# Kernel tuning notes

Measured on AMD Instinct MI355X. Metric: run time of the kernel, lower is better.

The kernel has to match this reference:

```python
import jax, jax.numpy as jnp
import numpy as np

NEG_INF = -jnp.inf


def setup_inputs() -> dict:
    key = jax.random.key(0)
    k1, k2, k3, k4 = jax.random.split(key, 4)
    B, V = 256, 128000
    logits = jax.random.normal(k1, (B, V), dtype=jnp.float32)
    temperatures = jax.random.uniform(k2, (B,), dtype=jnp.float32, minval=0.5, maxval=1.5)
    top_ks = jax.random.randint(k3, (B,), 0, 1024, dtype=jnp.int32)
    top_ps = jax.random.uniform(k4, (B,), dtype=jnp.float32)
    return {"logits": logits, "temperatures": temperatures, "top_ks": top_ks, "top_ps": top_ps}


def _filtered_logits(logits, temperatures, top_ks, top_ps):
    # Faithful vectorized version of the per-row torch loops.
    B, V = logits.shape
    x = logits.astype(jnp.float32) / temperatures[:, None]

    # Sort each row descending once; reuse for top-k and top-p.
    order = jnp.argsort(-x, axis=-1)                       # [B, V] desc indices
    sorted_x = jnp.take_along_axis(x, order, axis=-1)      # [B, V]
    ranks = jnp.arange(V)[None, :]                         # [1, V]

    # top-k: active only when 0 < k < V (matches torch branch)
    k = top_ks[:, None].astype(jnp.int32)
    topk_active = (k > 0) & (k < V)
    keep_k = jnp.where(topk_active, ranks < k, True)
    sorted_x = jnp.where(keep_k, sorted_x, NEG_INF)

    # top-p on softmax of top-k-filtered logits. Softmax is order-preserving,
    # so sorted probs == softmax of sorted (filtered) logits.
    sorted_probs = jax.nn.softmax(sorted_x, axis=-1)
    cumsum = jnp.cumsum(sorted_probs, axis=-1)
    p = top_ps[:, None]
    cutoff = jnp.sum(cumsum <= p, axis=-1, keepdims=True)  # (cumsum<=p).sum()
    cutoff = jnp.where(cutoff < V, cutoff + 1, cutoff)     # include next token
    topp_active = (p > 0.0) & (p < 1.0)
    keep_p = jnp.where(topp_active, ranks < cutoff, True)
    sorted_x = jnp.where(keep_p, sorted_x, NEG_INF)

    # Unsort back to original token order.
    inv = jnp.argsort(order, axis=-1)
    return jnp.take_along_axis(sorted_x, inv, axis=-1)


def reference(logits, temperatures, top_ks, top_ps):
    x = _filtered_logits(logits, temperatures, top_ks, top_ps)
    probs = jax.nn.softmax(x, axis=-1)
    # Gumbel-max style sampling: argmax(probs / Exp(1)) (torch .exponential_ trick)
    e = jax.random.exponential(jax.random.key(42), probs.shape, dtype=jnp.float32)
    e = jnp.maximum(e, 1e-10)
    return jnp.argmax(probs / e, axis=-1)
```

## Files before the change

kernel.cpp:

```cpp
#include <hip/hip_runtime.h>
#include <stdint.h>

#define VV 128000
#define BLOCK 1024
#define NB 4096
#define CAP 4096
#define THR 2.0f
#define U0  0xC0000000u
#define MSEL 2048

typedef unsigned long long ull;

__device__ __forceinline__ uint32_t rotl32(uint32_t x, int r){ return (x << r) | (x >> (32 - r)); }

__device__ __forceinline__ float exp_noise(uint32_t f){
  const uint32_t ks0 = 0u, ks1 = 42u, ks2 = 0x1BD11BDAu ^ 0u ^ 42u;
  uint32_t x0 = 0u + ks0;
  uint32_t x1 = f + ks1;
#define R1(r) { x0 += x1; x1 = rotl32(x1, r); x1 ^= x0; }
  R1(13) R1(15) R1(26) R1(6)   x0 += ks1; x1 += ks2 + 1u;
  R1(17) R1(29) R1(16) R1(24)  x0 += ks2; x1 += ks0 + 2u;
  R1(13) R1(15) R1(26) R1(6)   x0 += ks0; x1 += ks1 + 3u;
  R1(17) R1(29) R1(16) R1(24)  x0 += ks1; x1 += ks2 + 4u;
  R1(13) R1(15) R1(26) R1(6)   x0 += ks2; x1 += ks0 + 5u;
#undef R1
  uint32_t bits = x0 ^ x1;
  float u = __uint_as_float((bits >> 9) | 0x3F800000u) - 1.0f;
  float e = -log1pf(-u);
  return fmaxf(e, 1e-10f);
}

__device__ __forceinline__ uint32_t fkey(float x){
  uint32_t u = __float_as_uint(x);
  return u ^ ((u & 0x80000000u) ? 0xFFFFFFFFu : 0x80000000u);
}
__device__ __forceinline__ float keyval(uint32_t k){
  uint32_t bits = (k & 0x80000000u) ? (k ^ 0x80000000u) : ~k;
  return __uint_as_float(bits);
}

__device__ void suffix_scan_u(uint32_t* h, uint32_t* tmp, int tid){
  const int base = tid * 4;
  uint32_t l0=h[base], l1=h[base+1], l2=h[base+2], l3=h[base+3];
  uint32_t s3=l3, s2=l2+s3, s1=l1+s2, s0=l0+s1;
  tmp[tid] = s0; __syncthreads();
  for (int d=1; d<BLOCK; d<<=1){
    uint32_t add = (tid+d<BLOCK) ? tmp[tid+d] : 0u;
    __syncthreads();
    tmp[tid] += add;
    __syncthreads();
  }
  uint32_t E = (tid+1<BLOCK) ? tmp[tid+1] : 0u;
  h[base]=s0+E; h[base+1]=s1+E; h[base+2]=s2+E; h[base+3]=s3+E;
  __syncthreads();
}
__device__ void suffix_scan_f(float* h, float* tmp, int tid){
  const int base = tid * 4;
  float l0=h[base], l1=h[base+1], l2=h[base+2], l3=h[base+3];
  float s3=l3, s2=l2+s3, s1=l1+s2, s0=l0+s1;
  tmp[tid] = s0; __syncthreads();
  for (int d=1; d<BLOCK; d<<=1){
    float add = (tid+d<BLOCK) ? tmp[tid+d] : 0.f;
    __syncthreads();
    tmp[tid] += add;
    __syncthreads();
  }
  float E = (tid+1<BLOCK) ? tmp[tid+1] : 0.f;
  h[base]=s0+E; h[base+1]=s1+E; h[base+2]=s2+E; h[base+3]=s3+E;
  __syncthreads();
}

__device__ uint32_t select_tth_smallest(uint32_t* a, int n, int t){
  for (int i=0;i<t;i++){
    int mi=i; uint32_t mv=a[i];
    for (int j=i+1;j<n;j++) if (a[j]<mv){ mv=a[j]; mi=j; }
    a[mi]=a[i]; a[i]=mv;
  }
  return a[t-1];
}

__device__ void bitonic_sort(ull* a, int N, int tid){
  for (int len=2; len<=N; len<<=1){
    for (int j=len>>1; j>0; j>>=1){
      for (int i=tid; i<N; i+=BLOCK){
        int l = i ^ j;
        if (l > i){
          ull x = a[i], y = a[l];
          bool asc = ((i & len) == 0);
          if (asc ? (x > y) : (x < y)){ a[i]=y; a[l]=x; }
        }
      }
      __syncthreads();
    }
  }
}

#define ROW4R_BEGIN \
    for (int c0 = tid; c0 < VV/4; c0 += BLOCK*4){ \
      float4 qv[4]; int cb[4]; bool gv[4]; \
      _Pragma("unroll") \
      for (int t=0;t<4;t++){ int cc = c0 + t*BLOCK; gv[t] = (cc < VV/4); cb[t] = cc*4; if (gv[t]) qv[t] = rp[cc]; } \
      _Pragma("unroll") \
      for (int t=0;t<4;t++) if (gv[t]){ \
        float vs[4] = {qv[t].x, qv[t].y, qv[t].z, qv[t].w}; \
        _Pragma("unroll") \
        for (int j=0;j<4;j++){ \
          uint32_t u = fkey(vs[j]); \
          uint32_t idx = (uint32_t)(cb[t]+j); \
          (void)idx;
#define ROW4R_END } } }

#define ROW4_BEGIN \
    for (int c0 = tid; c0 < VV/4; c0 += BLOCK*4){ \
      float4 qv[4]; int cb[4]; bool gv[4]; \
      _Pragma("unroll") \
      for (int t=0;t<4;t++){ int cc = c0 + t*BLOCK; gv[t] = (cc < VV/4); cb[t] = cc*4; if (gv[t]) qv[t] = rp[cc]; } \
      _Pragma("unroll") \
      for (int t=0;t<4;t++) if (gv[t]){ \
        float xs[4] = {qv[t].x, qv[t].y, qv[t].z, qv[t].w}; \
        _Pragma("unroll") \
        for (int j=0;j<4;j++){ \
          float x = xs[j]/T; \
          uint32_t u = fkey(x); \
          uint32_t idx = (uint32_t)(cb[t]+j); \
          (void)idx;
#define ROW4_END } } }

__global__ __launch_bounds__(BLOCK) void sampler_kernel(
    const float* __restrict__ logits, const float* __restrict__ temps,
    const int* __restrict__ topks, const float* __restrict__ topps,
    int* __restrict__ out)
{
  __shared__ __align__(16) uint8_t SM[102400];
  uint32_t* h4    = (uint32_t*)SM;
  ull*      cand  = (ull*)SM;
  uint32_t* h2    = (uint32_t*)(SM + 32*1024);
  ull*      sort2 = (ull*)(SM + 48*1024);
  ull*      gcand = (ull*)SM;
  uint32_t* hc    = (uint32_t*)(SM + 32*1024);
  ull*      sel   = (ull*)(SM + 48*1024);
  float*    S     = (float*)SM;
  float*    wf    = (float*)(SM + 16*1024);
  uint32_t* wu    = (uint32_t*)(SM + 64*1024);
  float*    tmpf  = (float*)(SM + 80*1024);
  uint32_t* tmpu  = (uint32_t*)(SM + 84*1024);
  float*    ck    = (float*)(SM + 88*1024);
  ull*      red   = (ull*)(SM + 92*1024);

  __shared__ int s_idx, s_n, s_n2, s_tk, s_ntk, s_tp, s_ntp, s_nf, s_ns;
  __shared__ uint32_t s_uk, s_idxk, s_up, s_idxp;
  __shared__ float s_m, s_Zk, s_Ztot;
  __shared__ ull s_K0;

  const int b   = blockIdx.x;
  const int tid = threadIdx.x;
  const float T = temps[b];
  const int   k = topks[b];
  const float p = topps[b];
  const float* row = logits + (size_t)b * VV;
  const float4* rp = reinterpret_cast<const float4*>(row);
  const bool topk_act = (k > 0) && (k < VV);
  const bool topp_act = (p > 0.0f) && (p < 1.0f);

  if (topk_act){
    {
      if (tid==0) s_nf = 0;
      __syncthreads();
      for (int c0 = tid; c0 < VV/4; c0 += BLOCK*4){
        float4 qv[4]; int cb[4]; bool gvv[4];
        #pragma unroll
        for (int t=0;t<4;t++){ int cc=c0+t*BLOCK; gvv[t]=(cc<VV/4); cb[t]=cc*4; if(gvv[t]) qv[t]=rp[cc]; }
        #pragma unroll
        for (int t=0;t<4;t++) if (gvv[t]){
          float vsx[4]={qv[t].x,qv[t].y,qv[t].z,qv[t].w};
          #pragma unroll
          for (int j=0;j<4;j++){
            if (vsx[j] >= THR){
              int pos = atomicAdd(&s_nf, 1);
              if (pos < CAP) gcand[pos] = (((ull)fkey(vsx[j]))<<32) | (ull)(uint32_t)(cb[t]+j);
            }
          }
        }
      }
      __syncthreads();
      const int nf = s_nf;
      bool ok = (nf >= k) && (nf <= CAP) && (k <= BLOCK);
      int m = 0; uint32_t gam = 0u;
      if (ok){
        for (int i=tid;i<NB;i+=BLOCK) hc[i]=0u;
        __syncthreads();
        for (int i=tid;i<nf;i+=BLOCK){
          uint32_t u2 = (uint32_t)(gcand[i]>>32);
          uint32_t bu = (u2 - U0) >> 12; if (bu > 4095u) bu = 4095u;
          atomicAdd(&hc[bu], 1u);
        }
        __syncthreads();
        suffix_scan_u(hc, tmpu, tid);
        if (tid==0) s_idx = 0;
        __syncthreads();
        for (int i=tid;i<NB;i+=BLOCK){
          uint32_t a  = hc[i];
          uint32_t nn = (i+1<NB) ? hc[i+1] : 0u;
          if (a >= (uint32_t)k && nn < (uint32_t)k) s_idx = i;
        }
        __syncthreads();
        gam = (uint32_t)s_idx;
        m = (int)hc[gam];
        ok = (m <= MSEL);
      }
      if (ok){
        if (tid==0) s_ns = 0;
        __syncthreads();
        for (int i=tid;i<nf;i+=BLOCK){
          ull e = gcand[i];
          uint32_t u2 = (uint32_t)(e>>32);
          uint32_t bu = (u2 - U0) >> 12; if (bu > 4095u) bu = 4095u;
          if (bu >= gam){
            int pos = atomicAdd(&s_ns, 1);
            sel[pos] = (e & 0xFFFFFFFF00000000ull) | (ull)(~(uint32_t)e);
          }
        }
        __syncthreads();
        ull K0 = (tid < m)       ? sel[tid]       : 0ull;
        ull K1 = (tid+BLOCK < m) ? sel[tid+BLOCK] : 0ull;
        int r0 = 0, r1 = 0;
        #pragma unroll 4
        for (int j=0;j<m;j++){
          ull Kj = sel[j];
          r0 += (Kj > K0);
          r1 += (Kj > K1);
        }
        if (tid < m && r0 == 0)       s_K0 = K0;
        if (tid+BLOCK < m && r1 == 0) s_K0 = K1;
        __syncthreads();
        const float xm = keyval((uint32_t)(s_K0>>32)) / T;
        float w0 = 0.f, w1 = 0.f;
        if (tid < m && r0 < k)       w0 = expf(keyval((uint32_t)(K0>>32))/T - xm);
        if (tid+BLOCK < m && r1 < k) w1 = expf(keyval((uint32_t)(K1>>32))/T - xm);
        ck[tid] = 0.f;
        __syncthreads();
        if (tid < m && r0 < k)       ck[r0] = w0;
        if (tid+BLOCK < m && r1 < k) ck[r1] = w1;
        __syncthreads();
        for (int d=BLOCK/2; d>0; d>>=1){
          if (tid < d) ck[tid] += ck[tid+d];
          __syncthreads();
        }
        if (tid==0) s_Ztot = ck[0];
        __syncthreads();
        const float Zk = s_Ztot;
        ck[tid] = 0.f;
        __syncthreads();
        if (tid < m && r0 < k)       ck[r0] = w0 / Zk;
        if (tid+BLOCK < m && r1 < k) ck[r1] = w1 / Zk;
        __syncthreads();
        for (int d=1; d<BLOCK; d<<=1){
          float add = (tid >= d) ? ck[tid-d] : 0.f;
          __syncthreads();
          ck[tid] += add;
          __syncthreads();
        }
        tmpu[tid] = (tid < k && ck[tid] <= p) ? 1u : 0u;
        __syncthreads();
        for (int d=BLOCK/2; d>0; d>>=1){
          if (tid < d) tmpu[tid] += tmpu[tid+d];
          __syncthreads();
        }
        int L;
        if (!topp_act) L = k;
        else { int c = (int)tmpu[0]; L = (c >= k) ? k : (c + 1); }
        red[tid] = 0ull;
        __syncthreads();
        if (tid < m && r0 < L){
          uint32_t idx0 = ~(uint32_t)K0;
          float q = w0 / exp_noise((uint32_t)b * (uint32_t)VV + idx0);
          red[r0] = (((ull)__float_as_uint(q)) << 32) | (uint32_t)K0;
        }
        if (tid+BLOCK < m && r1 < L){
          uint32_t idx1 = ~(uint32_t)K1;
          float q = w1 / exp_noise((uint32_t)b * (uint32_t)VV + idx1);
          red[r1] = (((ull)__float_as_uint(q)) << 32) | (uint32_t)K1;
        }
        __syncthreads();
        for (int d=BLOCK/2; d>0; d>>=1){
          if (tid < d){ ull o = red[tid+d]; if (o > red[tid]) red[tid] = o; }
          __syncthreads();
        }
        if (tid==0) out[b] = (int)(~(uint32_t)(red[0] & 0xFFFFFFFFull));
        return;
      }
      __syncthreads();
    }

    for (int i=tid;i<4*NB;i+=BLOCK) h4[i]=0u;
    __syncthreads();
    ROW4R_BEGIN
      atomicAdd(&h4[((u>>20)<<2) | (uint32_t)(tid&3)], 1u);
    ROW4R_END
    __syncthreads();
    for (int i=tid;i<NB;i+=BLOCK)
      wu[i] = h4[(i<<2)] + h4[(i<<2)|1] + h4[(i<<2)|2] + h4[(i<<2)|3];
    __syncthreads();
    suffix_scan_u(wu, tmpu, tid);
    if (tid==0) s_idx = 0;
    __syncthreads();
    for (int i=tid;i<NB;i+=BLOCK){
      uint32_t a  = wu[i];
      uint32_t nn = (i+1<NB) ? wu[i+1] : 0u;
      if (a >= (uint32_t)k && nn < (uint32_t)k) s_idx = i;
    }
    __syncthreads();
    const uint32_t beta = (uint32_t)s_idx;
    const int n = (int)wu[beta];
    const uint32_t c_above = (beta+1<NB) ? wu[beta+1] : 0u;
    if (n <= CAP){
      if (tid==0) s_n = 0;
      __syncthreads();
      ROW4R_BEGIN
        if ((u>>20) >= beta){
          int pos = atomicAdd(&s_n, 1);
          cand[pos] = (((ull)(~u))<<32) | idx;
        }
      ROW4R_END
      __syncthreads();
      ull* srt; int m;
      if (n <= 1024){ srt = cand; m = n; }
      else {
        for (int i=tid;i<NB;i+=BLOCK) h2[i]=0u;
        __syncthreads();
        for (int i=tid;i<n;i+=BLOCK){
          uint32_t u2 = ~(uint32_t)(cand[i]>>32);
          if ((u2>>20) == beta) atomicAdd(&h2[(u2>>8)&0xFFFu], 1u);
        }
        __syncthreads();
        suffix_scan_u(h2, tmpu, tid);
        const uint32_t kr = (uint32_t)k - c_above;
        if (tid==0) s_idx = 0;
        __syncthreads();
        for (int i=tid;i<NB;i+=BLOCK){
          uint32_t a  = h2[i];
          uint32_t nn = (i+1<NB) ? h2[i+1] : 0u;
          if (a >= kr && nn < kr) s_idx = i;
        }
        __syncthreads();
        const uint32_t gam = (uint32_t)s_idx;
        const int np = (int)(c_above + h2[gam]);
        if (np <= 1024){
          if (tid==0) s_n2 = 0;
          __syncthreads();
          const uint32_t cut24 = (beta<<12) | gam;
          for (int i=tid;i<n;i+=BLOCK){
            ull e = cand[i];
            uint32_t u2 = ~(uint32_t)(e>>32);
            if ((u2>>8) >= cut24){
              int pos = atomicAdd(&s_n2, 1);
              sort2[pos] = e;
            }
          }
          __syncthreads();
          srt = sort2; m = np;
        } else { srt = cand; m = n; }
      }
      int N = 2; while (N < m) N <<= 1;
      for (int i=tid;i<N;i+=BLOCK) if (i >= m) srt[i] = 0xFFFFFFFFFFFFFFFFull;
      __syncthreads();
      bitonic_sort(srt, N, tid);
      const int kk = k;
      const float xm = keyval(~(uint32_t)(srt[0]>>32)) / T;
      float w = 0.f; uint32_t myidx = 0u;
      if (tid < kk){
        ull e = srt[tid];
        myidx = (uint32_t)e;
        float xv = keyval(~(uint32_t)(e>>32)) / T;
        w = expf(xv - xm);
      }
      ck[tid] = w; __syncthreads();
      for (int d=BLOCK/2; d>0; d>>=1){
        if (tid < d) ck[tid] += ck[tid+d];
        __syncthreads();
      }
      if (tid==0) s_Ztot = ck[0];
      __syncthreads();
      const float Zk = s_Ztot;
      ck[tid] = w / Zk; __syncthreads();
      for (int d=1; d<BLOCK; d<<=1){
        float add = (tid >= d) ? ck[tid-d] : 0.f;
        __syncthreads();
        ck[tid] += add;
        __syncthreads();
      }
      tmpu[tid] = (tid < kk && ck[tid] <= p) ? 1u : 0u;
      __syncthreads();
      for (int d=BLOCK/2; d>0; d>>=1){
        if (tid < d) tmpu[tid] += tmpu[tid+d];
        __syncthreads();
      }
      int L;
      if (!topp_act) L = kk;
      else { int c = (int)tmpu[0]; L = (c >= kk) ? kk : (c + 1); }
      ull best = 0ull;
      if (tid < L){
        float q = w / exp_noise((uint32_t)b * (uint32_t)VV + myidx);
        best = (((ull)__float_as_uint(q)) << 32) | (uint32_t)(~myidx);
      }
      red[tid] = best; __syncthreads();
      for (int d=BLOCK/2; d>0; d>>=1){
        if (tid < d){ ull o = red[tid+d]; if (o > red[tid]) red[tid] = o; }
        __syncthreads();
      }
      if (tid==0) out[b] = (int)(~(uint32_t)(red[0] & 0xFFFFFFFFull));
      return;
    }
    __syncthreads();
  }

  for (int i=tid;i<NB;i+=BLOCK){ S[i]=0.f; wu[i]=0u; }
  __syncthreads();
  float lmax = -3.4e38f;
  ROW4_BEGIN
    lmax = fmaxf(lmax, x);
    atomicAdd(&wu[u>>20], 1u);
    atomicAdd(&S[u>>20], expf(x));
  ROW4_END
  tmpf[tid] = lmax; __syncthreads();
  for (int d=BLOCK/2; d>0; d>>=1){
    if (tid < d) tmpf[tid] = fmaxf(tmpf[tid], tmpf[tid+d]);
    __syncthreads();
  }
  if (tid==0) s_m = tmpf[0];
  __syncthreads();
  suffix_scan_u(wu, tmpu, tid);
  suffix_scan_f(S,  tmpf, tid);

  uint32_t uk = 0u, idxk = 0xFFFFFFFFu;
  int bk1 = -1;
  if (topk_act){
    if (tid==0) s_idx = 0;
    __syncthreads();
    for (int i=tid;i<NB;i+=BLOCK){
      uint32_t a  = wu[i];
      uint32_t nn = (i+1<NB) ? wu[i+1] : 0u;
      if (a >= (uint32_t)k && nn < (uint32_t)k) s_idx = i;
    }
    __syncthreads();
    bk1 = s_idx;
    const uint32_t c_above1 = (bk1+1<NB) ? wu[bk1+1] : 0u;
    const float    M_above1 = (bk1+1<NB) ? S[bk1+1]  : 0.f;
    __syncthreads();
    for (int i=tid;i<NB;i+=BLOCK){ wu[i]=0u; wf[i]=0.f; }
    __syncthreads();
    ROW4_BEGIN
      if ((int)(u>>20) == bk1){
        atomicAdd(&wu[(u>>8)&0xFFFu], 1u);
        atomicAdd(&wf[(u>>8)&0xFFFu], expf(x));
      }
    ROW4_END
    __syncthreads();
    suffix_scan_u(wu, tmpu, tid);
    suffix_scan_f(wf, tmpf, tid);
    if (tid==0) s_idx = 0;
    __syncthreads();
    for (int i=tid;i<NB;i+=BLOCK){
      uint32_t a  = c_above1 + wu[i];
      uint32_t nn = c_above1 + ((i+1<NB) ? wu[i+1] : 0u);
      if (a >= (uint32_t)k && nn < (uint32_t)k) s_idx = i;
    }
    __syncthreads();
    const int bk2 = s_idx;
    const uint32_t c_above2 = c_above1 + ((bk2+1<NB) ? wu[bk2+1] : 0u);
    const float    M_above2 = M_above1 + ((bk2+1<NB) ? wf[bk2+1] : 0.f);
    __syncthreads();
    if (tid < 256){ wu[tid]=0u; wf[tid]=0.f; }
    __syncthreads();
    const uint32_t top24k = (((uint32_t)bk1)<<12) | (uint32_t)bk2;
    ROW4_BEGIN
      if ((u>>8) == top24k){
        atomicAdd(&wu[u & 0xFFu], 1u);
        atomicAdd(&wf[u & 0xFFu], expf(x));
      }
    ROW4_END
    __syncthreads();
    if (tid==0){
      uint32_t r = 0u; float mr = 0.f; int b3 = 0;
      for (int i=255;i>=0;--i){
        if (c_above2 + r + wu[i] >= (uint32_t)k){ b3 = i; break; }
        r += wu[i]; mr += wf[i];
      }
      const uint32_t cgt = c_above2 + r;
      const float mgt = M_above2 + mr;
      const int nt = (int)wu[b3];
      const int tk = k - (int)cgt;
      s_uk  = (((uint32_t)bk1)<<20) | (((uint32_t)bk2)<<8) | (uint32_t)b3;
      s_tk  = tk; s_ntk = nt;
      s_Zk  = mgt + (float)tk * expf(keyval(s_uk));
      s_n   = 0;
    }
    __syncthreads();
    uk = s_uk;
    if (s_tk < s_ntk){
      ROW4_BEGIN
        if (u == uk){
          int pos = atomicAdd(&s_n, 1);
          if (pos < NB) wu[pos] = idx;
        }
      ROW4_END
      __syncthreads();
      if (tid==0){
        int n2 = min(s_n, NB);
        int t  = min(s_tk, n2);
        s_idxk = select_tth_smallest(wu, n2, t);
      }
      __syncthreads();
      idxk = s_idxk;
    }
  }
  const float Zk = topk_act ? s_Zk : S[0];

  uint32_t up = 0u, idxp = 0xFFFFFFFFu;
  const float tgt = p * Zk;
  const bool pall = (!topp_act) || (tgt >= Zk);
  if (!pall){
    if (tid==0) s_idx = -2;
    __syncthreads();
    for (int i=tid;i<NB;i+=BLOCK){
      if (i > bk1){
        float a  = S[i];
        float nn = (i+1<NB) ? S[i+1] : 0.f;
        if (a > tgt && nn <= tgt) s_idx = i;
      }
    }
    __syncthreads();
    int bp1 = (s_idx >= 0) ? s_idx : bk1;
    if (bp1 < 0) bp1 = 0;
    const float Mab = (bp1+1<NB) ? S[bp1+1] : 0.f;
    __syncthreads();
    for (int i=tid;i<NB;i+=BLOCK) wf[i]=0.f;
    __syncthreads();
    ROW4_BEGIN
      if ((int)(u>>20) == bp1){
        bool kk_ok = (!topk_act) || (u > uk) || (u == uk && idx <= idxk);
        if (kk_ok) atomicAdd(&wf[(u>>8)&0xFFFu], expf(x));
      }
    ROW4_END
    __syncthreads();
    suffix_scan_f(wf, tmpf, tid);
    if (tid==0) s_idx = -2;
    __syncthreads();
    for (int i=tid;i<NB;i+=BLOCK){
      float a  = Mab + wf[i];
      float nn = Mab + ((i+1<NB) ? wf[i+1] : 0.f);
      if (a > tgt && nn <= tgt) s_idx = i;
    }
    __syncthreads();
    int bp2;
    if (s_idx >= 0){ bp2 = s_idx; }
    else {
      if (tid==0) s_idx = NB;
      __syncthreads();
      for (int i=tid;i<NB;i+=BLOCK){
        float a  = wf[i];
        float nn = (i+1<NB) ? wf[i+1] : 0.f;
        if (a > nn) atomicMin(&s_idx, i);
      }
      __syncthreads();
      bp2 = (s_idx < NB) ? s_idx : 0;
    }
    const float Mab2 = Mab + ((bp2+1<NB) ? wf[bp2+1] : 0.f);
    __syncthreads();
    if (tid < 256){ wf[tid]=0.f; wu[tid]=0u; }
    __syncthreads();
    const uint32_t top24p = (((uint32_t)bp1)<<12) | (uint32_t)bp2;
    ROW4_BEGIN
      if ((u>>8) == top24p){
        bool kk_ok = (!topk_act) || (u > uk) || (u == uk && idx <= idxk);
        if (kk_ok){
          atomicAdd(&wf[u & 0xFFu], expf(x));
          atomicAdd(&wu[u & 0xFFu], 1u);
        }
      }
    ROW4_END
    __syncthreads();
    if (tid==0){
      float run = 0.f; int b3 = -1; float mgt = 0.f;
      for (int i=255;i>=0;--i){
        float sufn = run; run += wf[i];
        if (Mab2 + run > tgt && Mab2 + sufn <= tgt){ b3 = i; mgt = Mab2 + sufn; break; }
      }
      if (b3 < 0){
        float run2 = 0.f;
        for (int i=255;i>=0;--i){
          if (wu[i] > 0u){ b3 = i; mgt = Mab2 + run2; }
          run2 += wf[i];
        }
        if (b3 < 0){ b3 = 0; mgt = Mab2; }
      }
      const uint32_t upv = (((uint32_t)bp1)<<20) | (((uint32_t)bp2)<<8) | (uint32_t)b3;
      const int ntp = (int)wu[b3];
      const float ev = expf(keyval(upv));
      int t = 0;
      for (int j=1;j<=ntp;j++){
        float before = mgt + (float)(j-1) * ev;
        if (before / Zk <= p) t++; else break;
      }
      if (t < 1) t = 1;
      s_up = upv; s_tp = t; s_ntp = ntp; s_n = 0;
    }
    __syncthreads();
    up = s_up;
    if (s_tp < s_ntp){
      ROW4_BEGIN
        if (u == up){
          bool kk_ok = (!topk_act) || (u > uk) || (u == uk && idx <= idxk);
          if (kk_ok){
            int pos = atomicAdd(&s_n, 1);
            if (pos < NB) wu[pos] = idx;
          }
        }
      ROW4_END
      __syncthreads();
      if (tid==0){
        int n2 = min(s_n, NB);
        int t  = min(s_tp, n2);
        s_idxp = select_tth_smallest(wu, n2, t);
      }
      __syncthreads();
      idxp = s_idxp;
    }
  }

  const float m  = s_m;
  const float Zs = Zk * expf(-m);
  ull best = 0ull;
  ROW4_BEGIN
    bool kk_ok = (!topk_act) || (u > uk) || (u == uk && idx <= idxk);
    bool kp_ok = pall || (u > up) || (u == up && idx <= idxp);
    if (kk_ok && kp_ok){
      float q = (expf(x - m) / Zs) / exp_noise((uint32_t)b * (uint32_t)VV + idx);
      ull pk = (((ull)__float_as_uint(q)) << 32) | (uint32_t)(~idx);
      best = (pk > best) ? pk : best;
    }
  ROW4_END
  red[tid] = best; __syncthreads();
  for (int d=BLOCK/2; d>0; d>>=1){
    if (tid < d){ ull o = red[tid+d]; if (o > red[tid]) red[tid] = o; }
    __syncthreads();
  }
  if (tid==0) out[b] = (int)(~(uint32_t)(red[0] & 0xFFFFFFFFull));
}

extern "C" void kernel_launch(void* const* d_in, const int* in_sizes, int n_in,
                              void* d_out, int out_size, void* d_ws, size_t ws_size,
                              hipStream_t stream) {
  (void)in_sizes; (void)n_in; (void)out_size; (void)d_ws; (void)ws_size;
  const float* logits = (const float*)d_in[0];
  const float* temps  = (const float*)d_in[1];
  const int*   ks     = (const int*)d_in[2];
  const float* ps     = (const float*)d_in[3];
  int* out = (int*)d_out;
  sampler_kernel<<<256, BLOCK, 0, stream>>>(logits, temps, ks, ps, out);
}
```

Baseline: 236.2 us.

## Split candidate gathering into a separate multi-block kernel with bucketed rank selection

Adds a pre-pass kernel that uses 16 blocks per row to scan logits and write values above a threshold into per-segment global workspace buffers. The main kernel then builds its histogram from these buffers, computes the suffix scan with wave shuffles, and scatters candidates into bucket order so each rank only compares within its own bucket instead of against all m candidates. The aim is to spread the first full-row scan across more blocks than one per row and to make the rank step cheaper. In exchange it adds a second launch and a global-memory round trip, and it depends on the workspace being large enough.

```diff
diff --git a/kernel.cpp b/kernel.cpp
--- a/kernel.cpp
+++ b/kernel.cpp
@@ -8,6 +8,9 @@
 #define THR 2.0f
 #define U0  0xC0000000u
 #define MSEL 2048
+#define NSEG 16
+#define CAPSEG 320
+#define F4SEG 2000
 
 typedef unsigned long long ull;
 
@@ -126,19 +129,53 @@
           (void)idx;
 #define ROW4_END } } }
 
+__global__ __launch_bounds__(256) void gather_kernel(
+    const float* __restrict__ logits, ull* __restrict__ g_cand,
+    uint32_t* __restrict__ g_cnt)
+{
+  const int bid = blockIdx.x;
+  const int row = bid >> 4, seg = bid & 15;
+  const int tid = threadIdx.x;
+  const float4* rp = reinterpret_cast<const float4*>(logits + (size_t)row * VV);
+  __shared__ ull buf[CAPSEG];
+  __shared__ int cnt;
+  if (tid==0) cnt = 0;
+  __syncthreads();
+  const int c1 = (seg+1)*F4SEG;
+  for (int c = seg*F4SEG + tid; c < c1; c += 256){
+    float4 q = rp[c];
+    float vs[4] = {q.x, q.y, q.z, q.w};
+    #pragma unroll
+    for (int j=0;j<4;j++){
+      if (vs[j] >= THR){
+        int pos = atomicAdd(&cnt, 1);
+        uint32_t idx = (uint32_t)(c*4 + j);
+        if (pos < CAPSEG) buf[pos] = (((ull)fkey(vs[j]))<<32) | (ull)(~idx);
+      }
+    }
+  }
+  __syncthreads();
+  const int n = min(cnt, CAPSEG);
+  ull* dst = g_cand + (size_t)row*(NSEG*CAPSEG) + seg*CAPSEG;
+  for (int i=tid;i<n;i+=256) dst[i] = buf[i];
+  if (tid==0) g_cnt[row*NSEG + seg] = (uint32_t)cnt;
+}
+
 __global__ __launch_bounds__(BLOCK) void sampler_kernel(
     const float* __restrict__ logits, const float* __restrict__ temps,
     const int* __restrict__ topks, const float* __restrict__ topps,
-    int* __restrict__ out)
+    int* __restrict__ out, const ull* __restrict__ g_cand,
+    const uint32_t* __restrict__ g_cnt, int use_ws)
 {
   __shared__ __align__(16) uint8_t SM[102400];
+  uint32_t* hist  = (uint32_t*)SM;
+  uint32_t* hsuf  = (uint32_t*)(SM + 16*1024);
+  ull*      srt2  = (ull*)(SM + 32*1024);
+  uint32_t* wtot  = (uint32_t*)(SM + 48*1024);
   uint32_t* h4    = (uint32_t*)SM;
   ull*      cand  = (ull*)SM;
   uint32_t* h2    = (uint32_t*)(SM + 32*1024);
   ull*      sort2 = (ull*)(SM + 48*1024);
-  ull*      gcand = (ull*)SM;
-  uint32_t* hc    = (uint32_t*)(SM + 32*1024);
-  ull*      sel   = (ull*)(SM + 48*1024);
   float*    S     = (float*)SM;
   float*    wf    = (float*)(SM + 16*1024);
   uint32_t* wu    = (uint32_t*)(SM + 64*1024);
@@ -147,7 +184,7 @@
   float*    ck    = (float*)(SM + 88*1024);
   ull*      red   = (ull*)(SM + 92*1024);
 
-  __shared__ int s_idx, s_n, s_n2, s_tk, s_ntk, s_tp, s_ntp, s_nf, s_ns;
+  __shared__ int s_idx, s_n, s_n2, s_tk, s_ntk, s_tp, s_ntp;
   __shared__ uint32_t s_uk, s_idxk, s_up, s_idxp;
   __shared__ float s_m, s_Zk, s_Ztot;
   __shared__ ull s_K0;
@@ -162,73 +199,94 @@
   const bool topk_act = (k > 0) && (k < VV);
   const bool topp_act = (p > 0.0f) && (p < 1.0f);
 
-  if (topk_act){
-    {
-      if (tid==0) s_nf = 0;
-      __syncthreads();
-      for (int c0 = tid; c0 < VV/4; c0 += BLOCK*4){
-        float4 qv[4]; int cb[4]; bool gvv[4];
+  if (topk_act && use_ws && k <= BLOCK){
+    int cs[NSEG]; int nf = 0; bool ovf = false;
+    const uint32_t* gc = g_cnt + b*NSEG;
+    #pragma unroll
+    for (int s=0;s<NSEG;s++){
+      int c = (int)gc[s];
+      if (c > CAPSEG) ovf = true;
+      c = min(c, CAPSEG);
+      cs[s] = c; nf += c;
+    }
+    if (!ovf && nf >= k){
+      const ull* gcd = g_cand + (size_t)b*(NSEG*CAPSEG);
+      for (int i=tid;i<NB;i+=BLOCK) hist[i]=0u;
+      __syncthreads();
+      for (int s=0;s<NSEG;s++){
+        for (int i=tid;i<cs[s];i+=BLOCK){
+          uint32_t u2 = (uint32_t)(gcd[s*CAPSEG+i]>>32);
+          uint32_t bu = (u2 - U0) >> 12; if (bu > 4095u) bu = 4095u;
+          atomicAdd(&hist[bu], 1u);
+        }
+      }
+      __syncthreads();
+      const int lane = tid & 63, wid = tid >> 6;
+      const int bb = tid*4;
+      uint32_t l0=hist[bb], l1=hist[bb+1], l2=hist[bb+2], l3=hist[bb+3];
+      uint32_t s3=l3, s2=l2+s3, s1=l1+s2, s0=l0+s1;
+      uint32_t v = s0;
+      #pragma unroll
+      for (int d=1; d<64; d<<=1){ uint32_t o=__shfl_down(v,d); if (lane+d<64) v += o; }
+      if (lane==0) wtot[wid] = v;
+      const uint32_t wexcl = v - s0;
+      __syncthreads();
+      if (wid==0){
+        uint32_t w = (lane<16) ? wtot[lane] : 0u;
+        uint32_t own = w;
         #pragma unroll
-        for (int t=0;t<4;t++){ int cc=c0+t*BLOCK; gvv[t]=(cc<VV/4); cb[t]=cc*4; if(gvv[t]) qv[t]=rp[cc]; }
-        #pragma unroll
-        for (int t=0;t<4;t++) if (gvv[t]){
-          float vsx[4]={qv[t].x,qv[t].y,qv[t].z,qv[t].w};
-          #pragma unroll
-          for (int j=0;j<4;j++){
-            if (vsx[j] >= THR){
-              int pos = atomicAdd(&s_nf, 1);
-              if (pos < CAP) gcand[pos] = (((ull)fkey(vsx[j]))<<32) | (ull)(uint32_t)(cb[t]+j);
+        for (int d=1; d<16; d<<=1){ uint32_t o=__shfl_down(w,d); if (lane+d<16) w += o; }
+        if (lane<16) wtot[lane] = w - own;
+      }
+      __syncthreads();
+      const uint32_t E = wtot[wid] + wexcl;
+      hsuf[bb]=s0+E; hsuf[bb+1]=s1+E; hsuf[bb+2]=s2+E; hsuf[bb+3]=s3+E;
+      if (tid==0) s_idx = 0;
+      __syncthreads();
+      #pragma unroll
+      for (int j=0;j<4;j++){
+        int i = bb+j;
+        uint32_t a  = hsuf[i];
+        uint32_t nn = (i < NB-1) ? hsuf[i+1] : 0u;
+        if (a >= (uint32_t)k && nn < (uint32_t)k) s_idx = i;
+      }
+      __syncthreads();
+      const int gam = s_idx;
+      const int m = (int)hsuf[gam];
+      if (m <= MSEL){
+        for (int s=0;s<NSEG;s++){
+          for (int i=tid;i<cs[s];i+=BLOCK){
+            ull e = gcd[s*CAPSEG+i];
+            uint32_t u2 = (uint32_t)(e>>32);
+            uint32_t bu = (u2 - U0) >> 12; if (bu > 4095u) bu = 4095u;
+            if ((int)bu >= gam){
+              uint32_t sub  = atomicSub(&hist[bu], 1u) - 1u;
+              uint32_t base = (bu < NB-1) ? hsuf[bu+1] : 0u;
+              srt2[base + sub] = e;
             }
           }
         }
-      }
-      __syncthreads();
-      const int nf = s_nf;
-      bool ok = (nf >= k) && (nf <= CAP) && (k <= BLOCK);
-      int m = 0; uint32_t gam = 0u;
-      if (ok){
-        for (int i=tid;i<NB;i+=BLOCK) hc[i]=0u;
-        __syncthreads();
-        for (int i=tid;i<nf;i+=BLOCK){
-          uint32_t u2 = (uint32_t)(gcand[i]>>32);
+        __syncthreads();
+        ull K0=0ull, K1=0ull; int r0=0, r1=0;
+        if (tid < m){
+          K0 = srt2[tid];
+          uint32_t u2 = (uint32_t)(K0>>32);
           uint32_t bu = (u2 - U0) >> 12; if (bu > 4095u) bu = 4095u;
-          atomicAdd(&hc[bu], 1u);
-        }
-        __syncthreads();
-        suffix_scan_u(hc, tmpu, tid);
-        if (tid==0) s_idx = 0;
-        __syncthreads();
-        for (int i=tid;i<NB;i+=BLOCK){
-          uint32_t a  = hc[i];
-          uint32_t nn = (i+1<NB) ? hc[i+1] : 0u;
-          if (a >= (uint32_t)k && nn < (uint32_t)k) s_idx = i;
-        }
-        __syncthreads();
-        gam = (uint32_t)s_idx;
-        m = (int)hc[gam];
-        ok = (m <= MSEL);
-      }
-      if (ok){
-        if (tid==0) s_ns = 0;
-        __syncthreads();
-        for (int i=tid;i<nf;i+=BLOCK){
-          ull e = gcand[i];
-          uint32_t u2 = (uint32_t)(e>>32);
+          uint32_t base = (bu < NB-1) ? hsuf[bu+1] : 0u;
+          uint32_t nb = hsuf[bu] - base;
+          int r = (int)base;
+          for (uint32_t q=0;q<nb;q++) r += (srt2[base+q] > K0);
+          r0 = r;
+        }
+        if (tid+BLOCK < m){
+          K1 = srt2[tid+BLOCK];
+          uint32_t u2 = (uint32_t)(K1>>32);
           uint32_t bu = (u2 - U0) >> 12; if (bu > 4095u) bu = 4095u;
-          if (bu >= gam){
-            int pos = atomicAdd(&s_ns, 1);
-            sel[pos] = (e & 0xFFFFFFFF00000000ull) | (ull)(~(uint32_t)e);
-          }
-        }
-        __syncthreads();
-        ull K0 = (tid < m)       ? sel[tid]       : 0ull;
-        ull K1 = (tid+BLOCK < m) ? sel[tid+BLOCK] : 0ull;
-        int r0 = 0, r1 = 0;
-        #pragma unroll 4
-        for (int j=0;j<m;j++){
-          ull Kj = sel[j];
-          r0 += (Kj > K0);
-          r1 += (Kj > K1);
+          uint32_t base = (bu < NB-1) ? hsuf[bu+1] : 0u;
+          uint32_t nb = hsuf[bu] - base;
+          int r = (int)base;
+          for (uint32_t q=0;q<nb;q++) r += (srt2[base+q] > K1);
+          r1 = r;
         }
         if (tid < m && r0 == 0)       s_K0 = K0;
         if (tid+BLOCK < m && r1 == 0) s_K0 = K1;
@@ -291,7 +349,9 @@
       }
       __syncthreads();
     }
-
+  }
+
+  if (topk_act){
     for (int i=tid;i<4*NB;i+=BLOCK) h4[i]=0u;
     __syncthreads();
     ROW4R_BEGIN
@@ -651,11 +711,23 @@
 extern "C" void kernel_launch(void* const* d_in, const int* in_sizes, int n_in,
                               void* d_out, int out_size, void* d_ws, size_t ws_size,
                               hipStream_t stream) {
-  (void)in_sizes; (void)n_in; (void)out_size; (void)d_ws; (void)ws_size;
+  (void)in_sizes; (void)n_in; (void)out_size;
   const float* logits = (const float*)d_in[0];
   const float* temps  = (const float*)d_in[1];
   const int*   ks     = (const int*)d_in[2];
   const float* ps     = (const float*)d_in[3];
   int* out = (int*)d_out;
-  sampler_kernel<<<256, BLOCK, 0, stream>>>(logits, temps, ks, ps, out);
-}
+
+  const size_t cnt_bytes  = 256 * NSEG * sizeof(uint32_t);
+  const size_t cand_bytes = (size_t)256 * NSEG * CAPSEG * sizeof(ull);
+  const size_t need = cnt_bytes + cand_bytes;
+
+  uint32_t* g_cnt  = (uint32_t*)d_ws;
+  ull*      g_cand = (ull*)((uint8_t*)d_ws + cnt_bytes);
+  const int use_ws = (d_ws != nullptr && ws_size >= need) ? 1 : 0;
+
+  if (use_ws)
+    gather_kernel<<<256*NSEG, 256, 0, stream>>>(logits, g_cand, g_cnt);
+  sampler_kernel<<<256, BLOCK, 0, stream>>>(logits, temps, ks, ps, out,
+                                            g_cand, g_cnt, use_ws);
+}
```

Result: faster. 212.0 us, median of 2 (-10.2%).
